# Optimization experiments

Measured on AMD Instinct MI355X. Metric: run time of the kernel, lower is better.

The kernel has to match this reference:

```python
import jax, jax.numpy as jnp
import numpy as np

MODEL_DIM = 1024
NUM_HEADS = 16
HEAD_DIM = MODEL_DIM // NUM_HEADS
BATCH = 2
SEQ = 2048


def setup_inputs() -> dict:
    key = jax.random.key(0)
    k1, k2, k3 = jax.random.split(key, 3)
    scale = 1.0 / np.sqrt(MODEL_DIM)
    return {
        "embeddings": jax.random.normal(k1, (BATCH, SEQ, MODEL_DIM), dtype=jnp.float32),
        "w_qkv": jax.random.normal(k2, (MODEL_DIM, 3 * MODEL_DIM), dtype=jnp.float32) * scale,
        "b_qkv": jnp.zeros((3 * MODEL_DIM,), dtype=jnp.float32),
        "w_out": jax.random.normal(k3, (MODEL_DIM, MODEL_DIM), dtype=jnp.float32) * scale,
        "b_out": jnp.zeros((MODEL_DIM,), dtype=jnp.float32),
    }


def reference(embeddings, w_qkv, b_qkv, w_out, b_out):
    B, S, _ = embeddings.shape
    # fused QKV projection: [B, S, 3*model_dim]
    qkv = embeddings @ w_qkv + b_qkv
    # -> [B, H, S, 3*head_dim], then split
    qkv = qkv.reshape(B, S, NUM_HEADS, 3 * HEAD_DIM).transpose(0, 2, 1, 3)
    q, k, v = jnp.split(qkv, 3, axis=-1)
    # scaled dot-product attention (full O(S^2) matrix, as in original)
    scale = 1.0 / jnp.sqrt(jnp.asarray(HEAD_DIM, dtype=embeddings.dtype))
    scores = jnp.einsum("bhqd,bhkd->bhqk", q, k) * scale
    attn = jax.nn.softmax(scores, axis=-1)
    ctx = jnp.einsum("bhqk,bhkd->bhqd", attn, v)
    # merge heads -> [B, S, model_dim], output projection
    ctx = ctx.transpose(0, 2, 1, 3).reshape(B, S, NUM_HEADS * HEAD_DIM)
    return ctx @ w_out + b_out
```

## Files before the change

### kernel.cpp

```cpp
#include <hip/hip_runtime.h>
#include <hip/hip_bf16.h>

#define MODEL 1024
#define NHEADS 16
#define HDIM 64
#define BATCH 2
#define SEQ 2048
#define NROWS (BATCH*SEQ)
#define QKVN (3*MODEL)
#define QSCALE 0.1803368801111204f

typedef __bf16 bf16x8 __attribute__((ext_vector_type(8)));
typedef float f32x4 __attribute__((ext_vector_type(4)));
typedef float f32x16 __attribute__((ext_vector_type(16)));

#define GLDS(g, l) __builtin_amdgcn_global_load_lds( \
    (const __attribute__((address_space(1))) void*)(g), \
    (__attribute__((address_space(3))) void*)(l), 16, 0, 0)

__device__ inline unsigned cvtpk(float a, float b) {
    unsigned la = __builtin_bit_cast(unsigned short, __float2bfloat16(a));
    unsigned hb = __builtin_bit_cast(unsigned short, __float2bfloat16(b));
    return la | (hb << 16);
}

__device__ inline size_t qk_fidx(int s, int d) {
    return (((size_t)((s >> 6) * 8 + ((s >> 5) & 1) * 4 + (d >> 4)) * 64)
            + (s & 31) + ((d >> 3) & 1) * 32) * 8 + (d & 7);
}
__device__ inline size_t v_fidx(int s, int d) {
    return (((size_t)((s >> 6) * 8 + (d >> 5) * 4 + ((s >> 4) & 3)) * 64)
            + (d & 31) + ((s >> 3) & 1) * 32) * 8 + (s & 7);
}


__global__ __launch_bounds__(256) void cvt_bf16_kernel(const float* __restrict__ in,
                                                       __hip_bfloat16* __restrict__ out, int n) {
    int i = (blockIdx.x * 256 + threadIdx.x) * 4;
    if (i < n) {
        float4 v = *(const float4*)(in + i);
        out[i + 0] = __float2bfloat16(v.x);
        out[i + 1] = __float2bfloat16(v.y);
        out[i + 2] = __float2bfloat16(v.z);
        out[i + 3] = __float2bfloat16(v.w);
    }
}

__global__ __launch_bounds__(256) void tcvt_kernel(const float* __restrict__ in,
                                                   __hip_bfloat16* __restrict__ out, int K, int N) {
    __shared__ float tile[32][33];
    int tx = threadIdx.x, ty = threadIdx.y;
    int n0 = blockIdx.x * 32, k0 = blockIdx.y * 32;
#pragma unroll
    for (int i = 0; i < 4; ++i)
        tile[ty + i * 8][tx] = in[(size_t)(k0 + ty + i * 8) * N + n0 + tx];
    __syncthreads();
#pragma unroll
    for (int i = 0; i < 4; ++i)
        out[(size_t)(n0 + ty + i * 8) * K + k0 + tx] = __float2bfloat16(tile[tx][ty + i * 8]);
}


template<int EPI>
__global__ __launch_bounds__(256) void gemm_bt_kernel(
    const __hip_bfloat16* __restrict__ A, const __hip_bfloat16* __restrict__ Bt,
    const float* __restrict__ bias, float* __restrict__ Cf,
    __hip_bfloat16* __restrict__ qb, __hip_bfloat16* __restrict__ kb,
    __hip_bfloat16* __restrict__ vb, int M, int N, int K)
{
    __shared__ __hip_bfloat16 As[128 * 32];
    __shared__ __hip_bfloat16 Bs[128 * 32];
    int tid = threadIdx.x;
    int lane = tid & 63, wv = tid >> 6;
    int wm = wv >> 1, wn = wv & 1;
    int g = lane >> 4, li = lane & 15;
    int row0 = blockIdx.y * 128, col0 = blockIdx.x * 128;

    f32x4 acc[4][4] = {};

    for (int kt = 0; kt < K; kt += 32) {
        __syncthreads();
#pragma unroll
        for (int s = 0; s < 2; ++s) {
            int idx = (s * 256 + tid) * 8;
            int r = idx >> 5, c = idx & 31;
            const __hip_bfloat16* ga = A + (size_t)(row0 + r) * K + kt + c;
            char* la = (char*)As + (size_t)(s * 4 + wv) * 1024;
            GLDS(ga, la);
            const __hip_bfloat16* gb = Bt + (size_t)(col0 + r) * K + kt + c;
            char* lb = (char*)Bs + (size_t)(s * 4 + wv) * 1024;
            GLDS(gb, lb);
        }
        __syncthreads();
        bf16x8 a[4], b[4];
#pragma unroll
        for (int m = 0; m < 4; ++m)
            a[m] = *(const bf16x8*)((const char*)As + (size_t)((wm * 64 + m * 16 + li) * 32 + g * 8) * 2);
#pragma unroll
        for (int n = 0; n < 4; ++n)
            b[n] = *(const bf16x8*)((const char*)Bs + (size_t)((wn * 64 + n * 16 + li) * 32 + g * 8) * 2);
#pragma unroll
        for (int m = 0; m < 4; ++m)
#pragma unroll
            for (int n = 0; n < 4; ++n)
                acc[m][n] = __builtin_amdgcn_mfma_f32_16x16x32_bf16(a[m], b[n], acc[m][n], 0, 0, 0);
    }

    if (EPI == 1) {
#pragma unroll
        for (int m = 0; m < 4; ++m) {
            int row = row0 + wm * 64 + m * 16 + g * 4;
#pragma unroll
            for (int n = 0; n < 4; ++n) {
                int col = col0 + wn * 64 + n * 16 + li;
                float bv = bias[col];
#pragma unroll
                for (int r = 0; r < 4; ++r)
                    Cf[(size_t)(row + r) * N + col] = acc[m][n][r] + bv;
            }
        }
    } else {
#pragma unroll
        for (int m = 0; m < 4; ++m)
#pragma unroll
            for (int r = 0; r < 4; ++r) {
                int row = row0 + wm * 64 + m * 16 + g * 4 + r;
                int b = row >> 11, s = row & 2047;
#pragma unroll
                for (int n = 0; n < 4; ++n) {
                    int col = col0 + wn * 64 + n * 16 + li;
                    float val = acc[m][n][r] + bias[col];
                    int h = col / 192;
                    int rem = col - h * 192;
                    int t = rem >> 6, d = rem & 63;
                    size_t base = (size_t)(b * NHEADS + h) * (SEQ * HDIM);
                    if (t == 0)
                        qb[base + qk_fidx(s, d)] = __float2bfloat16(val * QSCALE);
                    else if (t == 1)
                        kb[base + qk_fidx(s, d)] = __float2bfloat16(val);
                    else
                        vb[base + v_fidx(s, d)] = __float2bfloat16(val);
                }
            }
    }
}


__global__ __launch_bounds__(512, 2) void attn_kernel(
    const __hip_bfloat16* __restrict__ qfb, const __hip_bfloat16* __restrict__ kfb,
    const __hip_bfloat16* __restrict__ vfb, __hip_bfloat16* __restrict__ ctx)
{
    int tid = threadIdx.x;
    int lane = tid & 63, w = tid >> 6;
    int qi = lane & 31, hi = lane >> 5;
    int bh = blockIdx.x;
    int b = bh >> 4, h = bh & 15;
    int q0 = blockIdx.y * 256 + w * 32;

    const bf16x8* QF = (const bf16x8*)qfb + (size_t)bh * 16384;
    const bf16x8* KF = (const bf16x8*)kfb + (size_t)bh * 16384;
    const bf16x8* VF = (const bf16x8*)vfb + (size_t)bh * 16384;

    bf16x8 qv[4];
    {
        int qt = q0 >> 6, qr2 = (q0 >> 5) & 1;
#pragma unroll
        for (int st = 0; st < 4; ++st)
            qv[st] = QF[(size_t)qt * 512 + (qr2 * 4 + st) * 64 + lane];
    }

    f32x16 o0 = {}, o1 = {};
    float m = -INFINITY, l = 0.f;

    bf16x8 kc[8], kn[8], vv[8];
#pragma unroll
    for (int f = 0; f < 8; ++f) kc[f] = KF[f * 64 + lane];

    for (int t = 0; t < 32; ++t) {
        __builtin_amdgcn_s_barrier();
#pragma unroll
        for (int f = 0; f < 8; ++f) vv[f] = VF[(size_t)t * 512 + f * 64 + lane];
        int tn = (t + 1) & 31;
#pragma unroll
        for (int f = 0; f < 8; ++f) kn[f] = KF[(size_t)tn * 512 + f * 64 + lane];

        f32x16 s0 = {}, s1 = {};
#pragma unroll
        for (int st = 0; st < 4; ++st) {
            s0 = __builtin_amdgcn_mfma_f32_32x32x16_bf16(kc[st], qv[st], s0, 0, 0, 0);
            s1 = __builtin_amdgcn_mfma_f32_32x32x16_bf16(kc[4 + st], qv[st], s1, 0, 0, 0);
        }

        float tm[8];
#pragma unroll
        for (int i = 0; i < 8; ++i)
            tm[i] = fmaxf(fmaxf(s0[i], s0[8 + i]), fmaxf(s1[i], s1[8 + i]));
#pragma unroll
        for (int i = 0; i < 4; ++i) tm[i] = fmaxf(tm[i], tm[4 + i]);
        float mx = fmaxf(fmaxf(tm[0], tm[1]), fmaxf(tm[2], tm[3]));
        mx = fmaxf(mx, __shfl_xor(mx, 32));
        float mn = fmaxf(m, mx);
        float al = exp2f(m - mn);
        m = mn;
#pragma unroll
        for (int i = 0; i < 16; ++i) s0[i] = exp2f(s0[i] - mn);
#pragma unroll
        for (int i = 0; i < 16; ++i) s1[i] = exp2f(s1[i] - mn);
        float ts[8];
#pragma unroll
        for (int i = 0; i < 8; ++i) ts[i] = (s0[i] + s0[8 + i]) + (s1[i] + s1[8 + i]);
#pragma unroll
        for (int i = 0; i < 4; ++i) ts[i] = ts[i] + ts[4 + i];
        float sum = (ts[0] + ts[1]) + (ts[2] + ts[3]);
        sum += __shfl_xor(sum, 32);
        l = l * al + sum;
#pragma unroll
        for (int i = 0; i < 16; ++i) { o0[i] *= al; o1[i] *= al; }

        bf16x8 pb[4];
#pragma unroll
        for (int ks = 0; ks < 4; ++ks) {
            const f32x16& sv = (ks < 2) ? s0 : s1;
            const int base = (ks & 1) * 8;
            unsigned t0 = cvtpk(sv[base + 0], sv[base + 1]);
            unsigned t1 = cvtpk(sv[base + 2], sv[base + 3]);
            unsigned u0 = cvtpk(sv[base + 4], sv[base + 5]);
            unsigned u1 = cvtpk(sv[base + 6], sv[base + 7]);
            unsigned t0s = __shfl_xor(t0, 32);
            unsigned t1s = __shfl_xor(t1, 32);
            unsigned u0s = __shfl_xor(u0, 32);
            unsigned u1s = __shfl_xor(u1, 32);
            union { unsigned u[4]; bf16x8 v; } pk;
            pk.u[0] = hi ? u0s : t0;
            pk.u[1] = hi ? u1s : t1;
            pk.u[2] = hi ? u0 : t0s;
            pk.u[3] = hi ? u1 : t1s;
            pb[ks] = pk.v;
        }

#pragma unroll
        for (int ks = 0; ks < 4; ++ks) {
            o0 = __builtin_amdgcn_mfma_f32_32x32x16_bf16(vv[ks], pb[ks], o0, 0, 0, 0);
            o1 = __builtin_amdgcn_mfma_f32_32x32x16_bf16(vv[4 + ks], pb[ks], o1, 0, 0, 0);
        }
#pragma unroll
        for (int f = 0; f < 8; ++f) kc[f] = kn[f];
    }

    float inv = 1.f / l;
    __hip_bfloat16* crow = ctx + ((size_t)(b * SEQ) + q0 + qi) * MODEL + h * HDIM;
#pragma unroll
    for (int rg = 0; rg < 4; ++rg) {
        uint2 pk0, pk1;
        pk0.x = cvtpk(o0[rg * 4 + 0] * inv, o0[rg * 4 + 1] * inv);
        pk0.y = cvtpk(o0[rg * 4 + 2] * inv, o0[rg * 4 + 3] * inv);
        pk1.x = cvtpk(o1[rg * 4 + 0] * inv, o1[rg * 4 + 1] * inv);
        pk1.y = cvtpk(o1[rg * 4 + 2] * inv, o1[rg * 4 + 3] * inv);
        *(uint2*)(crow + rg * 8 + hi * 4) = pk0;
        *(uint2*)(crow + 32 + rg * 8 + hi * 4) = pk1;
    }
}


extern "C" void kernel_launch(void* const* d_in, const int* in_sizes, int n_in,
                              void* d_out, int out_size, void* d_ws, size_t ws_size,
                              hipStream_t stream) {
    const float* emb = (const float*)d_in[0];
    const float* w_qkv = (const float*)d_in[1];
    const float* b_qkv = (const float*)d_in[2];
    const float* w_out = (const float*)d_in[3];
    const float* b_out = (const float*)d_in[4];
    float* out = (float*)d_out;
    char* ws = (char*)d_ws;

    __hip_bfloat16* Xb    = (__hip_bfloat16*)(ws);
    __hip_bfloat16* Wqkvt = (__hip_bfloat16*)(ws + ((size_t)8  << 20));
    __hip_bfloat16* Woutt = (__hip_bfloat16*)(ws + ((size_t)14 << 20));
    __hip_bfloat16* qbuf  = (__hip_bfloat16*)(ws + ((size_t)16 << 20));
    __hip_bfloat16* kbuf  = (__hip_bfloat16*)(ws + ((size_t)24 << 20));
    __hip_bfloat16* vbuf  = (__hip_bfloat16*)(ws + ((size_t)32 << 20));
    __hip_bfloat16* ctx   = (__hip_bfloat16*)(ws + ((size_t)40 << 20));

    cvt_bf16_kernel<<<4096, 256, 0, stream>>>(emb, Xb, NROWS * MODEL);
    tcvt_kernel<<<dim3(QKVN / 32, MODEL / 32), dim3(32, 8), 0, stream>>>(w_qkv, Wqkvt, MODEL, QKVN);
    tcvt_kernel<<<dim3(MODEL / 32, MODEL / 32), dim3(32, 8), 0, stream>>>(w_out, Woutt, MODEL, MODEL);

    gemm_bt_kernel<0><<<dim3(QKVN / 128, NROWS / 128), 256, 0, stream>>>(
        Xb, Wqkvt, b_qkv, nullptr, qbuf, kbuf, vbuf, NROWS, QKVN, MODEL);

    attn_kernel<<<dim3(BATCH * NHEADS, SEQ / 256), 512, 0, stream>>>(qbuf, kbuf, vbuf, ctx);

    gemm_bt_kernel<1><<<dim3(MODEL / 128, NROWS / 128), 256, 0, stream>>>(
        ctx, Woutt, b_out, out, nullptr, nullptr, nullptr, NROWS, MODEL, MODEL);
}
```

Baseline: 228.1 us.

## Split KV range across waves, fuse prep kernels, lazy softmax rescale

The attention kernel now uses 64-query blocks of 4 waves, where two waves split the KV sequence in half per query group and merge partial softmax states through shared memory. This raises the grid from 256 to 1024 blocks for better CU occupancy. It also skips the online-softmax rescale unless the running max grows by more than 8, uses a native packed bf16 conversion instruction, halves the cross-lane shuffles when packing P, and drops K prefetch double-buffering. The three conversion and transpose kernels are merged into one launch. K/V traffic rises per query and the merge adds LDS work and barriers.

```diff
diff --git a/kernel.cpp b/kernel.cpp
--- a/kernel.cpp
+++ b/kernel.cpp
@@ -18,10 +18,10 @@
     (const __attribute__((address_space(1))) void*)(g), \
     (__attribute__((address_space(3))) void*)(l), 16, 0, 0)
 
-__device__ inline unsigned cvtpk(float a, float b) {
-    unsigned la = __builtin_bit_cast(unsigned short, __float2bfloat16(a));
-    unsigned hb = __builtin_bit_cast(unsigned short, __float2bfloat16(b));
-    return la | (hb << 16);
+__device__ inline unsigned cvtpk(float lo, float hi) {
+    unsigned r;
+    asm("v_cvt_pk_bf16_f32 %0, %1, %2" : "=v"(r) : "v"(lo), "v"(hi));
+    return r;
 }
 
 __device__ inline size_t qk_fidx(int s, int d) {
@@ -34,23 +34,31 @@
 }
 
 
-__global__ __launch_bounds__(256) void cvt_bf16_kernel(const float* __restrict__ in,
-                                                       __hip_bfloat16* __restrict__ out, int n) {
-    int i = (blockIdx.x * 256 + threadIdx.x) * 4;
-    if (i < n) {
-        float4 v = *(const float4*)(in + i);
-        out[i + 0] = __float2bfloat16(v.x);
-        out[i + 1] = __float2bfloat16(v.y);
-        out[i + 2] = __float2bfloat16(v.z);
-        out[i + 3] = __float2bfloat16(v.w);
-    }
-}
-
-__global__ __launch_bounds__(256) void tcvt_kernel(const float* __restrict__ in,
-                                                   __hip_bfloat16* __restrict__ out, int K, int N) {
+__global__ __launch_bounds__(256) void prep_kernel(
+    const float* __restrict__ emb, __hip_bfloat16* __restrict__ Xb,
+    const float* __restrict__ wqkv, __hip_bfloat16* __restrict__ Wqkvt,
+    const float* __restrict__ wout, __hip_bfloat16* __restrict__ Woutt)
+{
     __shared__ float tile[32][33];
-    int tx = threadIdx.x, ty = threadIdx.y;
-    int n0 = blockIdx.x * 32, k0 = blockIdx.y * 32;
+    int bid = blockIdx.x, tid = threadIdx.x;
+    if (bid < 4096) {
+        int i = (bid * 256 + tid) * 4;
+        float4 v = *(const float4*)(emb + i);
+        Xb[i + 0] = __float2bfloat16(v.x);
+        Xb[i + 1] = __float2bfloat16(v.y);
+        Xb[i + 2] = __float2bfloat16(v.z);
+        Xb[i + 3] = __float2bfloat16(v.w);
+        return;
+    }
+    const float* in; __hip_bfloat16* out; int K, N, n0, k0;
+    if (bid < 7168) {
+        int t = bid - 4096; in = wqkv; out = Wqkvt; K = MODEL; N = QKVN;
+        n0 = (t % 96) * 32; k0 = (t / 96) * 32;
+    } else {
+        int t = bid - 7168; in = wout; out = Woutt; K = MODEL; N = MODEL;
+        n0 = (t & 31) * 32; k0 = (t >> 5) * 32;
+    }
+    int tx = tid & 31, ty = tid >> 5;
 #pragma unroll
     for (int i = 0; i < 4; ++i)
         tile[ty + i * 8][tx] = in[(size_t)(k0 + ty + i * 8) * N + n0 + tx];
@@ -146,43 +154,37 @@
 }
 
 
-__global__ __launch_bounds__(512, 2) void attn_kernel(
+__global__ __launch_bounds__(256, 3) void attn_kernel(
     const __hip_bfloat16* __restrict__ qfb, const __hip_bfloat16* __restrict__ kfb,
     const __hip_bfloat16* __restrict__ vfb, __hip_bfloat16* __restrict__ ctx)
 {
+    __shared__ float Ms[2][64], Ls[2][64], Os[2][32][64];
     int tid = threadIdx.x;
     int lane = tid & 63, w = tid >> 6;
+    int qg = w & 1, kvh = w >> 1;
     int qi = lane & 31, hi = lane >> 5;
     int bh = blockIdx.x;
     int b = bh >> 4, h = bh & 15;
-    int q0 = blockIdx.y * 256 + w * 32;
+    int q0 = blockIdx.y * 64 + qg * 32;
 
     const bf16x8* QF = (const bf16x8*)qfb + (size_t)bh * 16384;
     const bf16x8* KF = (const bf16x8*)kfb + (size_t)bh * 16384;
     const bf16x8* VF = (const bf16x8*)vfb + (size_t)bh * 16384;
 
     bf16x8 qv[4];
-    {
-        int qt = q0 >> 6, qr2 = (q0 >> 5) & 1;
-#pragma unroll
-        for (int st = 0; st < 4; ++st)
-            qv[st] = QF[(size_t)qt * 512 + (qr2 * 4 + st) * 64 + lane];
-    }
+#pragma unroll
+    for (int st = 0; st < 4; ++st)
+        qv[st] = QF[(size_t)blockIdx.y * 512 + (qg * 4 + st) * 64 + lane];
 
     f32x16 o0 = {}, o1 = {};
     float m = -INFINITY, l = 0.f;
 
-    bf16x8 kc[8], kn[8], vv[8];
-#pragma unroll
-    for (int f = 0; f < 8; ++f) kc[f] = KF[f * 64 + lane];
-
-    for (int t = 0; t < 32; ++t) {
+    for (int tt = 0; tt < 16; ++tt) {
+        int t = kvh * 16 + tt;
         __builtin_amdgcn_s_barrier();
-#pragma unroll
-        for (int f = 0; f < 8; ++f) vv[f] = VF[(size_t)t * 512 + f * 64 + lane];
-        int tn = (t + 1) & 31;
-#pragma unroll
-        for (int f = 0; f < 8; ++f) kn[f] = KF[(size_t)tn * 512 + f * 64 + lane];
+        bf16x8 kc[8];
+#pragma unroll
+        for (int f = 0; f < 8; ++f) kc[f] = KF[(size_t)t * 512 + f * 64 + lane];
 
         f32x16 s0 = {}, s1 = {};
 #pragma unroll
@@ -191,6 +193,10 @@
             s1 = __builtin_amdgcn_mfma_f32_32x32x16_bf16(kc[4 + st], qv[st], s1, 0, 0, 0);
         }
 
+        bf16x8 vv[8];
+#pragma unroll
+        for (int f = 0; f < 8; ++f) vv[f] = VF[(size_t)t * 512 + f * 64 + lane];
+
         float tm[8];
 #pragma unroll
         for (int i = 0; i < 8; ++i)
@@ -199,13 +205,18 @@
         for (int i = 0; i < 4; ++i) tm[i] = fmaxf(tm[i], tm[4 + i]);
         float mx = fmaxf(fmaxf(tm[0], tm[1]), fmaxf(tm[2], tm[3]));
         mx = fmaxf(mx, __shfl_xor(mx, 32));
-        float mn = fmaxf(m, mx);
-        float al = exp2f(m - mn);
-        m = mn;
-#pragma unroll
-        for (int i = 0; i < 16; ++i) s0[i] = exp2f(s0[i] - mn);
-#pragma unroll
-        for (int i = 0; i < 16; ++i) s1[i] = exp2f(s1[i] - mn);
+        if (__any(mx - m > 8.0f)) {
+            float mn = fmaxf(m, mx);
+            float al = __builtin_amdgcn_exp2f(m - mn);
+            m = mn;
+            l *= al;
+#pragma unroll
+            for (int i = 0; i < 16; ++i) { o0[i] *= al; o1[i] *= al; }
+        }
+#pragma unroll
+        for (int i = 0; i < 16; ++i) s0[i] = __builtin_amdgcn_exp2f(s0[i] - m);
+#pragma unroll
+        for (int i = 0; i < 16; ++i) s1[i] = __builtin_amdgcn_exp2f(s1[i] - m);
         float ts[8];
 #pragma unroll
         for (int i = 0; i < 8; ++i) ts[i] = (s0[i] + s0[8 + i]) + (s1[i] + s1[8 + i]);
@@ -213,9 +224,7 @@
         for (int i = 0; i < 4; ++i) ts[i] = ts[i] + ts[4 + i];
         float sum = (ts[0] + ts[1]) + (ts[2] + ts[3]);
         sum += __shfl_xor(sum, 32);
-        l = l * al + sum;
-#pragma unroll
-        for (int i = 0; i < 16; ++i) { o0[i] *= al; o1[i] *= al; }
+        l += sum;
 
         bf16x8 pb[4];
 #pragma unroll
@@ -226,15 +235,13 @@
             unsigned t1 = cvtpk(sv[base + 2], sv[base + 3]);
             unsigned u0 = cvtpk(sv[base + 4], sv[base + 5]);
             unsigned u1 = cvtpk(sv[base + 6], sv[base + 7]);
-            unsigned t0s = __shfl_xor(t0, 32);
-            unsigned t1s = __shfl_xor(t1, 32);
-            unsigned u0s = __shfl_xor(u0, 32);
-            unsigned u1s = __shfl_xor(u1, 32);
+            unsigned ra = __shfl_xor(hi ? t0 : u0, 32);
+            unsigned rb = __shfl_xor(hi ? t1 : u1, 32);
             union { unsigned u[4]; bf16x8 v; } pk;
-            pk.u[0] = hi ? u0s : t0;
-            pk.u[1] = hi ? u1s : t1;
-            pk.u[2] = hi ? u0 : t0s;
-            pk.u[3] = hi ? u1 : t1s;
+            pk.u[0] = hi ? ra : t0;
+            pk.u[1] = hi ? rb : t1;
+            pk.u[2] = hi ? u0 : ra;
+            pk.u[3] = hi ? u1 : rb;
             pb[ks] = pk.v;
         }
 
@@ -243,21 +250,37 @@
             o0 = __builtin_amdgcn_mfma_f32_32x32x16_bf16(vv[ks], pb[ks], o0, 0, 0, 0);
             o1 = __builtin_amdgcn_mfma_f32_32x32x16_bf16(vv[4 + ks], pb[ks], o1, 0, 0, 0);
         }
-#pragma unroll
-        for (int f = 0; f < 8; ++f) kc[f] = kn[f];
-    }
-
-    float inv = 1.f / l;
-    __hip_bfloat16* crow = ctx + ((size_t)(b * SEQ) + q0 + qi) * MODEL + h * HDIM;
-#pragma unroll
-    for (int rg = 0; rg < 4; ++rg) {
-        uint2 pk0, pk1;
-        pk0.x = cvtpk(o0[rg * 4 + 0] * inv, o0[rg * 4 + 1] * inv);
-        pk0.y = cvtpk(o0[rg * 4 + 2] * inv, o0[rg * 4 + 3] * inv);
-        pk1.x = cvtpk(o1[rg * 4 + 0] * inv, o1[rg * 4 + 1] * inv);
-        pk1.y = cvtpk(o1[rg * 4 + 2] * inv, o1[rg * 4 + 3] * inv);
-        *(uint2*)(crow + rg * 8 + hi * 4) = pk0;
-        *(uint2*)(crow + 32 + rg * 8 + hi * 4) = pk1;
+    }
+
+    __syncthreads();
+    if (kvh == 1) {
+        Ms[qg][lane] = m; Ls[qg][lane] = l;
+#pragma unroll
+        for (int i = 0; i < 16; ++i) { Os[qg][i][lane] = o0[i]; Os[qg][16 + i][lane] = o1[i]; }
+    }
+    __syncthreads();
+    if (kvh == 0) {
+        float m2 = Ms[qg][lane], l2 = Ls[qg][lane];
+        float mn = fmaxf(m, m2);
+        float a = __builtin_amdgcn_exp2f(m - mn);
+        float b2 = __builtin_amdgcn_exp2f(m2 - mn);
+        float linv = 1.f / (l * a + l2 * b2);
+        __hip_bfloat16* crow = ctx + ((size_t)(b * SEQ) + q0 + qi) * MODEL + h * HDIM;
+#pragma unroll
+        for (int rg = 0; rg < 4; ++rg) {
+            float c0[4], c1[4];
+#pragma unroll
+            for (int e = 0; e < 4; ++e) {
+                int i = rg * 4 + e;
+                c0[e] = (o0[i] * a + Os[qg][i][lane] * b2) * linv;
+                c1[e] = (o1[i] * a + Os[qg][16 + i][lane] * b2) * linv;
+            }
+            uint2 pk0, pk1;
+            pk0.x = cvtpk(c0[0], c0[1]); pk0.y = cvtpk(c0[2], c0[3]);
+            pk1.x = cvtpk(c1[0], c1[1]); pk1.y = cvtpk(c1[2], c1[3]);
+            *(uint2*)(crow + rg * 8 + hi * 4) = pk0;
+            *(uint2*)(crow + 32 + rg * 8 + hi * 4) = pk1;
+        }
     }
 }
 
@@ -281,14 +304,12 @@
     __hip_bfloat16* vbuf  = (__hip_bfloat16*)(ws + ((size_t)32 << 20));
     __hip_bfloat16* ctx   = (__hip_bfloat16*)(ws + ((size_t)40 << 20));
 
-    cvt_bf16_kernel<<<4096, 256, 0, stream>>>(emb, Xb, NROWS * MODEL);
-    tcvt_kernel<<<dim3(QKVN / 32, MODEL / 32), dim3(32, 8), 0, stream>>>(w_qkv, Wqkvt, MODEL, QKVN);
-    tcvt_kernel<<<dim3(MODEL / 32, MODEL / 32), dim3(32, 8), 0, stream>>>(w_out, Woutt, MODEL, MODEL);
+    prep_kernel<<<8192, 256, 0, stream>>>(emb, Xb, w_qkv, Wqkvt, w_out, Woutt);
 
     gemm_bt_kernel<0><<<dim3(QKVN / 128, NROWS / 128), 256, 0, stream>>>(
         Xb, Wqkvt, b_qkv, nullptr, qbuf, kbuf, vbuf, NROWS, QKVN, MODEL);
 
-    attn_kernel<<<dim3(BATCH * NHEADS, SEQ / 256), 512, 0, stream>>>(qbuf, kbuf, vbuf, ctx);
+    attn_kernel<<<dim3(BATCH * NHEADS, SEQ / 64), 256, 0, stream>>>(qbuf, kbuf, vbuf, ctx);
 
     gemm_bt_kernel<1><<<dim3(MODEL / 128, NROWS / 128), 256, 0, stream>>>(
         ctx, Woutt, b_out, out, nullptr, nullptr, nullptr, NROWS, MODEL, MODEL);
```

After: 211.4 us. 1.08x faster.
